# Kernel tuning notes

Measured on AMD Instinct MI355X. Metric: run time of the kernel, lower is better.

The kernel has to match this reference:

```python
import jax, jax.numpy as jnp
import numpy as np

B, N, EMBED, CHEB_K, INP, HID = 32, 8192, 16, 2, 2, 64


def setup_inputs() -> dict:
    key = jax.random.key(0)
    k1, k2, k3, k4 = jax.random.split(key, 4)
    return {
        "x": jax.random.normal(k1, (B, N, INP), dtype=jnp.float32),
        "adj": jax.random.normal(k2, (N, EMBED), dtype=jnp.float32),
        "weights_pool": jax.random.normal(k3, (EMBED, CHEB_K, INP, HID), dtype=jnp.float32) * 0.1,
        "bias_pool": jax.random.normal(k4, (EMBED, HID), dtype=jnp.float32) * 0.1,
    }


def reference(x, adj, weights_pool, bias_pool):
    n = adj.shape[0]
    cheb_k = weights_pool.shape[1]
    # adaptive adjacency: row-softmax of relu(E E^T)
    ADJ = jax.nn.softmax(jax.nn.relu(adj @ adj.T), axis=1)  # [n, n]
    support_set = [jnp.eye(n, dtype=x.dtype), ADJ]
    for k in range(2, cheb_k):  # Chebyshev recursion (fixed small k)
        support_set.append(2.0 * ADJ @ support_set[-1] - support_set[-2])
    supports = jnp.stack(support_set, axis=0)  # [k, n, n]
    # node-adaptive weights / bias
    weights = jnp.einsum("nd,dkio->nkio", adj, weights_pool)  # [n,k,inp,hid]
    bias = adj @ bias_pool  # [n, hid]
    # graph propagation, directly in bnkc layout (fuses the permute)
    x_g = jnp.einsum("knm,bmc->bnkc", supports, x)  # [b,n,k,inp]
    out = jnp.einsum("bnki,nkio->bno", x_g, weights) + bias  # [b,n,hid]
    return out
```

## Files before the change

kernel.cpp:

```cpp
#include <hip/hip_runtime.h>

#define NN 8192
#define BB 32
#define EMB 16
#define HID 64
#define MS 16

typedef __attribute__((ext_vector_type(8))) short bf16x8;
typedef __attribute__((ext_vector_type(4))) float f32x4;

static __device__ inline unsigned short f2b(float f) {
    union { float f; unsigned u; } v; v.f = f;
    return (unsigned short)((v.u + 0x7fffu + ((v.u >> 16) & 1u)) >> 16);
}

static __device__ inline unsigned packbf(unsigned e_even, unsigned e_odd) {
#if __has_builtin(__builtin_amdgcn_perm)
    return __builtin_amdgcn_perm(e_odd, e_even, 0x07060302u);
#else
    return (e_odd & 0xFFFF0000u) | (e_even >> 16);
#endif
}

__global__ void k_build(const float* __restrict__ x, const float* __restrict__ adj,
                        const float* __restrict__ wp, const float* __restrict__ bp,
                        short* __restrict__ VTf, short* __restrict__ Afrag,
                        short* __restrict__ adjS, unsigned short* __restrict__ WbufB) {
    const int t = threadIdx.x;
    const int bx = blockIdx.x;
    if (bx < 256) {
        const int c = bx;
        const int u = t >> 6, lane = t & 63, l = lane & 15, q = lane >> 4;
        const int j = 16 * u + l, b = j >> 1, ch = j & 1;
        const int m0 = 32 * c + 8 * q;
        const float* xp = x + (size_t)b * (NN * 2) + m0 * 2;
        uint4 d;
        unsigned dd[4];
#pragma unroll
        for (int i = 0; i < 4; ++i) {
            float4 xx = *(const float4*)(xp + 4 * i);
            float v0 = ch ? xx.y : xx.x;
            float v1 = ch ? xx.w : xx.z;
            dd[i] = (unsigned)f2b(v0) | ((unsigned)f2b(v1) << 16);
        }
        d.x = dd[0]; d.y = dd[1]; d.z = dd[2]; d.w = dd[3];
        *(uint4*)(VTf + ((size_t)(c * 4 + u) * 64 + lane) * 8) = d;
    } else if (bx < 384) {
        const int cc = t >> 7, tt = t & 127;
        const int c = (bx - 256) * 2 + cc;
        const int h = tt >> 6, lane = tt & 63, l = lane & 15, q = lane >> 4;
        const int row = 32 * c + 8 * (l >> 2) + (l & 3) + 4 * h;
        const float* ap = adj + (size_t)row * EMB + (q & 1) * 8;
        float4 a0 = *(const float4*)(ap);
        float4 a1 = *(const float4*)(ap + 4);
        uint4 d;
        d.x = (unsigned)f2b(a0.x) | ((unsigned)f2b(a0.y) << 16);
        d.y = (unsigned)f2b(a0.z) | ((unsigned)f2b(a0.w) << 16);
        d.z = (unsigned)f2b(a1.x) | ((unsigned)f2b(a1.y) << 16);
        d.w = (unsigned)f2b(a1.z) | ((unsigned)f2b(a1.w) << 16);
        *(uint4*)(Afrag + ((size_t)(c * 2 + h) * 64 + lane) * 8) = d;
    } else if (bx < 512) {
        const float L2E = 1.4426950408889634f;
        int idx = (bx - 384) * 256 + t;
        float4 aa = *(const float4*)(adj + (size_t)idx * 4);
        uint2 us;
        us.x = (unsigned)f2b(aa.x * L2E) | ((unsigned)f2b(aa.y * L2E) << 16);
        us.y = (unsigned)f2b(aa.z * L2E) | ((unsigned)f2b(aa.w * L2E) << 16);
        *(uint2*)(adjS + (size_t)idx * 4) = us;
    } else {
        const int nl = t >> 4, og = t & 15;
        const int n = (bx - 512) * 16 + nl;
        const float4* wp4 = (const float4*)wp;
        const float4* bp4 = (const float4*)bp;
        float an[EMB];
#pragma unroll
        for (int d = 0; d < EMB; ++d) an[d] = adj[n * EMB + d];
        float4 w[5];
#pragma unroll
        for (int c = 0; c < 5; ++c) { w[c].x = w[c].y = w[c].z = w[c].w = 0.f; }
#pragma unroll
        for (int d = 0; d < EMB; ++d) {
            float a = an[d];
#pragma unroll
            for (int c = 0; c < 4; ++c) {
                float4 p = wp4[(d * 4 + c) * 16 + og];
                w[c].x += a * p.x; w[c].y += a * p.y; w[c].z += a * p.z; w[c].w += a * p.w;
            }
            float4 pb = bp4[d * 16 + og];
            w[4].x += a * pb.x; w[4].y += a * pb.y; w[4].z += a * pb.z; w[4].w += a * pb.w;
        }
#pragma unroll
        for (int c = 0; c < 5; ++c) {
            ushort4 pk;
            pk.x = f2b(w[c].x); pk.y = f2b(w[c].y); pk.z = f2b(w[c].z); pk.w = f2b(w[c].w);
            *(ushort4*)(WbufB + (size_t)n * 320 + c * 64 + og * 4) = pk;
        }
    }
}

__launch_bounds__(256, 4)
__global__ void k_prop(const short* __restrict__ Afrag, const short* __restrict__ adjS,
                       const short* __restrict__ VTf,
                       short* __restrict__ ynum, float* __restrict__ den) {
    const int t = threadIdx.x;
    const int wv = t >> 6;
    const int lane = t & 63;
    const int l = lane & 15;
    const int q = lane >> 4;
    const int n0 = blockIdx.x * 128 + wv * 32;
    const int cbeg = blockIdx.y * (NN / MS / 32);
    const int cend = cbeg + (NN / MS / 32);

    bf16x8 Bn[2];
    bf16x8 zv = {0, 0, 0, 0, 0, 0, 0, 0};
#pragma unroll
    for (int s = 0; s < 2; ++s) {
        const short* src = adjS + (size_t)(n0 + 16 * s + l) * EMB + (q & 1) * 8;
        bf16x8 v = *(const bf16x8*)src;
        Bn[s] = (q < 2) ? v : zv;
    }
    const short one = (short)0x3F80;
    bf16x8 ones = {one, one, one, one, one, one, one, one};

    f32x4 acc[4][2];
    f32x4 dacc[2];
#pragma unroll
    for (int u = 0; u < 4; ++u)
#pragma unroll
        for (int s = 0; s < 2; ++s) { acc[u][s][0] = acc[u][s][1] = acc[u][s][2] = acc[u][s][3] = 0.f; }
#pragma unroll
    for (int s = 0; s < 2; ++s) { dacc[s][0] = dacc[s][1] = dacc[s][2] = dacc[s][3] = 0.f; }

    const short* Ap = Afrag + (size_t)lane * 8;
    const short* Vp = VTf + (size_t)lane * 8;

    bf16x8 aCur0 = *(const bf16x8*)(Ap + (size_t)cbeg * 1024);
    bf16x8 aCur1 = *(const bf16x8*)(Ap + (size_t)cbeg * 1024 + 512);

    for (int cg = cbeg; cg < cend; ++cg) {
        bf16x8 v0 = *(const bf16x8*)(Vp + (size_t)cg * 2048);
        bf16x8 v1 = *(const bf16x8*)(Vp + (size_t)cg * 2048 + 512);
        bf16x8 v2 = *(const bf16x8*)(Vp + (size_t)cg * 2048 + 1024);
        bf16x8 v3 = *(const bf16x8*)(Vp + (size_t)cg * 2048 + 1536);
        const int cgn = (cg + 1 < cend) ? cg + 1 : cbeg;
        bf16x8 aN0 = *(const bf16x8*)(Ap + (size_t)cgn * 1024);
        bf16x8 aN1 = *(const bf16x8*)(Ap + (size_t)cgn * 1024 + 512);

        f32x4 z = {0.f, 0.f, 0.f, 0.f};
        f32x4 S0[2], S1[2];
#pragma unroll
        for (int s = 0; s < 2; ++s) {
            S0[s] = __builtin_amdgcn_mfma_f32_16x16x32_bf16(aCur0, Bn[s], z, 0, 0, 0);
            S1[s] = __builtin_amdgcn_mfma_f32_16x16x32_bf16(aCur1, Bn[s], z, 0, 0, 0);
        }
#pragma unroll
        for (int s = 0; s < 2; ++s) {
            unsigned w0[4], w1[4];
#pragma unroll
            for (int r = 0; r < 4; ++r) {
                union { float f; unsigned u; } p0, p1;
                p0.f = __builtin_amdgcn_exp2f(fmaxf(S0[s][r], 0.f));
                p1.f = __builtin_amdgcn_exp2f(fmaxf(S1[s][r], 0.f));
                w0[r] = p0.u;
                w1[r] = p1.u;
            }
            union { bf16x8 v; unsigned d[4]; } pf;
            pf.d[0] = packbf(w0[0], w0[1]);
            pf.d[1] = packbf(w0[2], w0[3]);
            pf.d[2] = packbf(w1[0], w1[1]);
            pf.d[3] = packbf(w1[2], w1[3]);
            acc[0][s] = __builtin_amdgcn_mfma_f32_16x16x32_bf16(v0, pf.v, acc[0][s], 0, 0, 0);
            acc[1][s] = __builtin_amdgcn_mfma_f32_16x16x32_bf16(v1, pf.v, acc[1][s], 0, 0, 0);
            acc[2][s] = __builtin_amdgcn_mfma_f32_16x16x32_bf16(v2, pf.v, acc[2][s], 0, 0, 0);
            acc[3][s] = __builtin_amdgcn_mfma_f32_16x16x32_bf16(v3, pf.v, acc[3][s], 0, 0, 0);
            dacc[s] = __builtin_amdgcn_mfma_f32_16x16x32_bf16(ones, pf.v, dacc[s], 0, 0, 0);
        }
        aCur0 = aN0;
        aCur1 = aN1;
    }

    short* yp = ynum + (size_t)blockIdx.y * NN * HID;
#pragma unroll
    for (int s = 0; s < 2; ++s) {
        const int n = n0 + 16 * s + l;
#pragma unroll
        for (int u = 0; u < 4; ++u) {
            union { float f; unsigned u; } a0, a1, a2, a3;
            a0.f = acc[u][s][0]; a1.f = acc[u][s][1]; a2.f = acc[u][s][2]; a3.f = acc[u][s][3];
            uint2 pk;
            pk.x = packbf(a0.u, a1.u);
            pk.y = packbf(a2.u, a3.u);
            *(uint2*)(yp + (size_t)n * HID + 16 * u + 4 * q) = pk;
        }
        if (q == 0) den[(size_t)blockIdx.y * NN + n] = dacc[s][0];
    }
}

__global__ void k_epi(const unsigned short* __restrict__ WbufB, const float* __restrict__ x,
                      const short* __restrict__ ynum, const float* __restrict__ den,
                      float* __restrict__ out) {
    const int nl = threadIdx.x >> 4, og = threadIdx.x & 15;
    const int n = blockIdx.x * 16 + nl;
    __shared__ float xl[16][68];
    __shared__ float yl[16][68];

    float4 W[5];
#pragma unroll
    for (int c = 0; c < 5; ++c) {
        ushort4 pw = *(const ushort4*)(WbufB + (size_t)n * 320 + c * 64 + og * 4);
        union { unsigned u; float f; } c0, c1, c2, c3;
        c0.u = (unsigned)pw.x << 16; c1.u = (unsigned)pw.y << 16;
        c2.u = (unsigned)pw.z << 16; c3.u = (unsigned)pw.w << 16;
        W[c].x = c0.f; W[c].y = c1.f; W[c].z = c2.f; W[c].w = c3.f;
    }

    float4 ysum; ysum.x = ysum.y = ysum.z = ysum.w = 0.f;
    float dsum = 0.f;
#pragma unroll
    for (int s = 0; s < MS; ++s) {
        ushort4 p = *(const ushort4*)(ynum + ((size_t)s * NN + n) * HID + og * 4);
        union { unsigned u; float f; } c0, c1, c2, c3;
        c0.u = (unsigned)p.x << 16; c1.u = (unsigned)p.y << 16;
        c2.u = (unsigned)p.z << 16; c3.u = (unsigned)p.w << 16;
        ysum.x += c0.f; ysum.y += c1.f; ysum.z += c2.f; ysum.w += c3.f;
        dsum += den[(size_t)s * NN + n];
    }
    float rden = 1.f / dsum;
    *(float4*)&yl[nl][og * 4] = make_float4(ysum.x * rden, ysum.y * rden, ysum.z * rden, ysum.w * rden);

    float2 x0 = *(const float2*)(x + ((size_t)(og * 2) * NN + n) * 2);
    float2 x1 = *(const float2*)(x + ((size_t)(og * 2 + 1) * NN + n) * 2);
    xl[nl][og * 4 + 0] = x0.x; xl[nl][og * 4 + 1] = x0.y;
    xl[nl][og * 4 + 2] = x1.x; xl[nl][og * 4 + 3] = x1.y;
    __syncthreads();

#pragma unroll 4
    for (int b = 0; b < BB; ++b) {
        float xb0 = xl[nl][2 * b], xb1 = xl[nl][2 * b + 1];
        float yb0 = yl[nl][2 * b], yb1 = yl[nl][2 * b + 1];
        f32x4 o4;
        o4[0] = xb0 * W[0].x + xb1 * W[1].x + yb0 * W[2].x + yb1 * W[3].x + W[4].x;
        o4[1] = xb0 * W[0].y + xb1 * W[1].y + yb0 * W[2].y + yb1 * W[3].y + W[4].y;
        o4[2] = xb0 * W[0].z + xb1 * W[1].z + yb0 * W[2].z + yb1 * W[3].z + W[4].z;
        o4[3] = xb0 * W[0].w + xb1 * W[1].w + yb0 * W[2].w + yb1 * W[3].w + W[4].w;
        __builtin_nontemporal_store(o4, (f32x4*)(out + ((size_t)b * NN + n) * HID + og * 4));
    }
}

extern "C" void kernel_launch(void* const* d_in, const int* in_sizes, int n_in,
                              void* d_out, int out_size, void* d_ws, size_t ws_size,
                              hipStream_t stream) {
    const float* x   = (const float*)d_in[0];
    const float* adj = (const float*)d_in[1];
    const float* wp  = (const float*)d_in[2];
    const float* bp  = (const float*)d_in[3];
    float* out = (float*)d_out;

    char* w = (char*)d_ws;
    short* VTf   = (short*)w;
    short* Afrag = VTf + (size_t)256 * 4 * 64 * 8;
    short* adjS  = Afrag + (size_t)256 * 2 * 64 * 8;
    unsigned short* WbufB = (unsigned short*)(adjS + (size_t)NN * EMB);
    short* ynum  = (short*)(WbufB + (size_t)NN * 320);
    float* den   = (float*)(ynum + (size_t)MS * NN * HID);

    k_build<<<1024, 256, 0, stream>>>(x, adj, wp, bp, VTf, Afrag, adjS, WbufB);
    k_prop<<<dim3(NN / 128, MS), 256, 0, stream>>>(Afrag, adjS, VTf, ynum, den);
    k_epi<<<NN / 16, 256, 0, stream>>>(WbufB, x, ynum, den, out);
}
```

Measured before the change: 121.4 us.

## Fuse propagation and epilogue kernels with in-block split-K reduction via shared memory

```diff
diff --git a/kernel.cpp b/kernel.cpp
--- a/kernel.cpp
+++ b/kernel.cpp
@@ -4,7 +4,6 @@
 #define BB 32
 #define EMB 16
 #define HID 64
-#define MS 16
 
 typedef __attribute__((ext_vector_type(8))) short bf16x8;
 typedef __attribute__((ext_vector_type(4))) float f32x4;
@@ -98,18 +97,24 @@
     }
 }
 
-__launch_bounds__(256, 4)
-__global__ void k_prop(const short* __restrict__ Afrag, const short* __restrict__ adjS,
-                       const short* __restrict__ VTf,
-                       short* __restrict__ ynum, float* __restrict__ den) {
+__launch_bounds__(512, 2)
+__global__ void k_fused(const short* __restrict__ Afrag, const short* __restrict__ adjS,
+                        const short* __restrict__ VTf,
+                        const unsigned short* __restrict__ WbufB, const float* __restrict__ x,
+                        float* __restrict__ out) {
     const int t = threadIdx.x;
     const int wv = t >> 6;
     const int lane = t & 63;
     const int l = lane & 15;
     const int q = lane >> 4;
-    const int n0 = blockIdx.x * 128 + wv * 32;
-    const int cbeg = blockIdx.y * (NN / MS / 32);
-    const int cend = cbeg + (NN / MS / 32);
+    const int n0 = blockIdx.x * 32;
+    const int cbeg = wv * 32;
+    const int cend = cbeg + 32;
+
+    __shared__ __align__(16) unsigned short ysl[8][32][68];
+    __shared__ float dsl[8][32];
+    __shared__ float xl[32][68];
+    __shared__ float ylf[32][68];
 
     bf16x8 Bn[2];
     bf16x8 zv = {0, 0, 0, 0, 0, 0, 0, 0};
@@ -179,10 +184,9 @@
         aCur1 = aN1;
     }
 
-    short* yp = ynum + (size_t)blockIdx.y * NN * HID;
 #pragma unroll
     for (int s = 0; s < 2; ++s) {
-        const int n = n0 + 16 * s + l;
+        const int nl_w = 16 * s + l;
 #pragma unroll
         for (int u = 0; u < 4; ++u) {
             union { float f; unsigned u; } a0, a1, a2, a3;
@@ -190,19 +194,14 @@
             uint2 pk;
             pk.x = packbf(a0.u, a1.u);
             pk.y = packbf(a2.u, a3.u);
-            *(uint2*)(yp + (size_t)n * HID + 16 * u + 4 * q) = pk;
-        }
-        if (q == 0) den[(size_t)blockIdx.y * NN + n] = dacc[s][0];
-    }
-}
-
-__global__ void k_epi(const unsigned short* __restrict__ WbufB, const float* __restrict__ x,
-                      const short* __restrict__ ynum, const float* __restrict__ den,
-                      float* __restrict__ out) {
-    const int nl = threadIdx.x >> 4, og = threadIdx.x & 15;
-    const int n = blockIdx.x * 16 + nl;
-    __shared__ float xl[16][68];
-    __shared__ float yl[16][68];
+            *(uint2*)&ysl[wv][nl_w][16 * u + 4 * q] = pk;
+        }
+        if (q == 0) dsl[wv][nl_w] = dacc[s][0];
+    }
+    __syncthreads();
+
+    const int nl = t >> 4, og = t & 15;
+    const int n = n0 + nl;
 
     float4 W[5];
 #pragma unroll
@@ -217,16 +216,16 @@
     float4 ysum; ysum.x = ysum.y = ysum.z = ysum.w = 0.f;
     float dsum = 0.f;
 #pragma unroll
-    for (int s = 0; s < MS; ++s) {
-        ushort4 p = *(const ushort4*)(ynum + ((size_t)s * NN + n) * HID + og * 4);
+    for (int s = 0; s < 8; ++s) {
+        ushort4 p = *(const ushort4*)&ysl[s][nl][og * 4];
         union { unsigned u; float f; } c0, c1, c2, c3;
         c0.u = (unsigned)p.x << 16; c1.u = (unsigned)p.y << 16;
         c2.u = (unsigned)p.z << 16; c3.u = (unsigned)p.w << 16;
         ysum.x += c0.f; ysum.y += c1.f; ysum.z += c2.f; ysum.w += c3.f;
-        dsum += den[(size_t)s * NN + n];
+        dsum += dsl[s][nl];
     }
     float rden = 1.f / dsum;
-    *(float4*)&yl[nl][og * 4] = make_float4(ysum.x * rden, ysum.y * rden, ysum.z * rden, ysum.w * rden);
+    *(float4*)&ylf[nl][og * 4] = make_float4(ysum.x * rden, ysum.y * rden, ysum.z * rden, ysum.w * rden);
 
     float2 x0 = *(const float2*)(x + ((size_t)(og * 2) * NN + n) * 2);
     float2 x1 = *(const float2*)(x + ((size_t)(og * 2 + 1) * NN + n) * 2);
@@ -237,7 +236,7 @@
 #pragma unroll 4
     for (int b = 0; b < BB; ++b) {
         float xb0 = xl[nl][2 * b], xb1 = xl[nl][2 * b + 1];
-        float yb0 = yl[nl][2 * b], yb1 = yl[nl][2 * b + 1];
+        float yb0 = ylf[nl][2 * b], yb1 = ylf[nl][2 * b + 1];
         f32x4 o4;
         o4[0] = xb0 * W[0].x + xb1 * W[1].x + yb0 * W[2].x + yb1 * W[3].x + W[4].x;
         o4[1] = xb0 * W[0].y + xb1 * W[1].y + yb0 * W[2].y + yb1 * W[3].y + W[4].y;
@@ -261,10 +260,7 @@
     short* Afrag = VTf + (size_t)256 * 4 * 64 * 8;
     short* adjS  = Afrag + (size_t)256 * 2 * 64 * 8;
     unsigned short* WbufB = (unsigned short*)(adjS + (size_t)NN * EMB);
-    short* ynum  = (short*)(WbufB + (size_t)NN * 320);
-    float* den   = (float*)(ynum + (size_t)MS * NN * HID);
 
     k_build<<<1024, 256, 0, stream>>>(x, adj, wp, bp, VTf, Afrag, adjS, WbufB);
-    k_prop<<<dim3(NN / 128, MS), 256, 0, stream>>>(Afrag, adjS, VTf, ynum, den);
-    k_epi<<<NN / 16, 256, 0, stream>>>(WbufB, x, ynum, den, out);
-}
+    k_fused<<<NN / 32, 512, 0, stream>>>(Afrag, adjS, VTf, WbufB, x, out);
+}
```

Result: faster. 116.6 us (-3.9%).
